# Performance work log

Measured on AMD Instinct MI355X. Metric: run time of the kernel, lower is better.

## Reference

```python
import jax, jax.numpy as jnp
import numpy as np

RADIX = 23                 # hidden_radix fixed-point fractional bits
SCALE = float(1 << RADIX)
F = 10                     # fractional bits used to quantize forget gates
FS = 1 << F
MAX_FORGET = 0.875
H = 512
D = H // 2
SLICE = 100
VOCAB = 32000
T, B = 512, 64
L = 2


def setup_inputs() -> dict:
    key = jax.random.key(0)
    ks = jax.random.split(key, 8)
    s = 0.06  # ~1/sqrt(768) init scale, keeps gates unsaturated
    return {
        "input_seq": jax.random.randint(ks[0], (T, B), 0, VOCAB),
        "lengths": jax.random.randint(ks[1], (B,), 1, T + 1),
        "emb": jax.random.normal(ks[2], (VOCAB, H), jnp.float32) * s,
        "Wz1": jax.random.normal(ks[3], (L, H + D, H), jnp.float32) * s,
        "bz1": jnp.zeros((L, H), jnp.float32),
        "Wg1": jax.random.normal(ks[4], (L, H + D, D), jnp.float32) * s,
        "bg1": jnp.zeros((L, D), jnp.float32),
        "Wz2": jax.random.normal(ks[5], (L, H + D, H), jnp.float32) * s,
        "bz2": jnp.zeros((L, H), jnp.float32),
        "Wg2": jax.random.normal(ks[6], (L, H + D, D), jnp.float32) * s,
        "bg2": jnp.zeros((L, D), jnp.float32),
    }


def _to_float(h_int):
    # ConvertToFloat: dequantize int fixed-point hidden (radix 23)
    return h_int.astype(jnp.float32) / SCALE


def _quant_gate(z):
    # restrict forgetting: z in [1 - max_forget, 1], then quantize to F frac bits
    z = MAX_FORGET * z + (1.0 - MAX_FORGET)
    return jnp.clip(jnp.floor(z * FS), 1, FS).astype(jnp.int32)


def _fixed_mul(h, zq):
    # exact floor(h * zq / 2**F) in int32 (no overflow): split h into hi/lo
    h_hi = h >> F               # arithmetic shift == floor division
    h_lo = h & (FS - 1)
    return h_hi * zq + ((h_lo * zq) >> F)


def _revgru_cell(x, h, Wz1, bz1, Wg1, bg1, Wz2, bz2, Wg2, bg2):
    # h: int32 [B, H] fixed-point hidden, split into reversible halves
    h1, h2 = h[:, :D], h[:, D:]
    h2f = _to_float(h2)
    zr1 = jax.nn.sigmoid(jnp.concatenate([x, h2f], 1) @ Wz1 + bz1)   # [B, H]
    zq1, r1 = _quant_gate(zr1[:, :D]), zr1[:, D:]
    z1f = zq1.astype(jnp.float32) / FS
    g1 = jnp.tanh(jnp.concatenate([x, r1 * h2f], 1) @ Wg1 + bg1)     # [B, D]
    h1 = _fixed_mul(h1, zq1) + jnp.round((1.0 - z1f) * g1 * SCALE).astype(jnp.int32)
    h1f = _to_float(h1)
    zr2 = jax.nn.sigmoid(jnp.concatenate([x, h1f], 1) @ Wz2 + bz2)
    zq2, r2 = _quant_gate(zr2[:, :D]), zr2[:, D:]
    z2f = zq2.astype(jnp.float32) / FS
    g2 = jnp.tanh(jnp.concatenate([x, r2 * h1f], 1) @ Wg2 + bg2)
    h2 = _fixed_mul(h2, zq2) + jnp.round((1.0 - z2f) * g2 * SCALE).astype(jnp.int32)
    return jnp.concatenate([h1, h2], 1)


def reference(input_seq, lengths, emb, Wz1, bz1, Wg1, bg1, Wz2, bz2, Wg2, bg2):
    input_seq = input_seq.astype(jnp.int32)
    xs = emb[input_seq]                                       # [T, B, H] (lockdropi p=0)
    mask = jnp.arange(T)[:, None] < lengths[None, :]          # [T, B]
    h0 = jnp.zeros((B, H), jnp.int32)
    cur = xs
    last_hiddens = []
    all_hs = None
    # stacked RNN: run each layer fully over time (equivalent to the t,l double loop)
    for l in range(L):
        def step(h, inp, l=l):
            x, m = inp
            hn = _revgru_cell(x, h, Wz1[l], bz1[l], Wg1[l], bg1[l],
                              Wz2[l], bz2[l], Wg2[l], bg2[l])
            hn = jnp.where(m[:, None], hn, h)                 # length masking
            return hn, hn
        hT, hs = jax.lax.scan(step, h0, (cur, mask))
        last_hiddens.append(hT)
        if l < L - 1:
            cur = _to_float(hs)                               # output_hidden (lockdroph p=0)
        else:
            all_hs = hs
    # saved_hiddens: top-layer hidden slice before each step plus final -> T+1 entries
    saved = jnp.concatenate([h0[None], all_hs], 0)[:, :, :SLICE]
    return jnp.stack(last_hiddens), saved
```

## Files before the change

### kernel.cpp

```cpp
#include <hip/hip_runtime.h>
#include <stdint.h>


typedef __attribute__((ext_vector_type(8))) short short8;
typedef __attribute__((ext_vector_type(4))) float floatx4;

#define MFMA16(a,b,c) __builtin_amdgcn_mfma_f32_16x16x32_bf16((a),(b),(c),0,0,0)

__device__ __forceinline__ short bf16_rne(float f) {
  uint32_t u = __float_as_uint(f);
  u += 0x7FFFu + ((u >> 16) & 1u);
  return (short)(u >> 16);
}
__device__ __forceinline__ float bf16f(short s) {
  return __uint_as_float(((uint32_t)(uint16_t)s) << 16);
}
__device__ __forceinline__ void st64(unsigned long long* p, unsigned long long v) {
  __hip_atomic_store(p, v, __ATOMIC_RELAXED, __HIP_MEMORY_SCOPE_AGENT);
}
__device__ __forceinline__ unsigned long long ld64(const unsigned long long* p) {
  return __hip_atomic_load(p, __ATOMIC_RELAXED, __HIP_MEMORY_SCOPE_AGENT);
}

#define SCALE_F 8388608.0f
#define INV_S   (1.0f/8388608.0f)

__device__ float g_X[50331648];
__device__ short g_WTh[2][786432];
__device__ short g_WTl[2][786432];
__device__ float g_biasL[2][1536];
__device__ unsigned long long g_ch[2][4][6][4096];
__device__ unsigned long long g_h0s[16777216];
__device__ unsigned long long g_x1r[3145728];
__device__ unsigned long long g_sent[2][4][4][8];
__device__ unsigned g_epoch;

__global__ void bump_epoch() { g_epoch = g_epoch + 1u; }

__global__ void prep_x(const float* __restrict__ Wz1, const float* __restrict__ bz1,
                       const float* __restrict__ Wg1, const float* __restrict__ bg1,
                       const float* __restrict__ Wz2, const float* __restrict__ bz2,
                       const float* __restrict__ Wg2, const float* __restrict__ bg2,
                       int layer, int* __restrict__ d_out, int zero_extra) {
  int idx = blockIdx.x * 256 + threadIdx.x;
  int k = idx / 1536;
  int c = idx - k * 1536;
  const float* W; const float* bb; int cc; int ncols;
  if (c < 512)       { W = Wz1; bb = bz1; cc = c;        ncols = 512; }
  else if (c < 768)  { W = Wg1; bb = bg1; cc = c - 512;  ncols = 256; }
  else if (c < 1280) { W = Wz2; bb = bz2; cc = c - 768;  ncols = 512; }
  else               { W = Wg2; bb = bg2; cc = c - 1280; ncols = 256; }
  float wv = W[(size_t)layer * 768 * ncols + (size_t)k * ncols + cc];
  short hi = bf16_rne(wv);
  short lo = bf16_rne(wv - bf16f(hi));
  g_WTh[layer][(size_t)c * 512 + k] = hi;
  g_WTl[layer][(size_t)c * 512 + k] = lo;
  if (k == 0) g_biasL[layer][c] = bb[layer * ncols + cc];
  if (zero_extra && idx < 6400) d_out[65536 + idx] = 0;
}

__global__ __launch_bounds__(256)
void gemmx_kernel(const int* __restrict__ seq, const float* __restrict__ emb) {
  __shared__ float At[128][36];
  __shared__ short Bhi[128][40];
  __shared__ short Blo[128][40];
  __shared__ int toks[128];
  int tid = threadIdx.x;
  int r0 = blockIdx.x * 128;
  int c0 = blockIdx.y * 128;
  if (tid < 128) toks[tid] = seq[r0 + tid];
  int lane = tid & 63;
  int wid = tid >> 6;
  int wm = wid & 1, wn = wid >> 1;
  int lm = lane & 15, lq = lane >> 4;
  floatx4 zero4 = {0.f, 0.f, 0.f, 0.f};
  floatx4 acc[4][4];
#pragma unroll
  for (int a = 0; a < 4; ++a)
#pragma unroll
    for (int b = 0; b < 4; ++b) acc[a][b] = zero4;
  __syncthreads();
  int am = tid >> 1;
  int ah = (tid & 1) * 16;
  const float* arow = emb + (size_t)toks[am] * 512;
  const short* bh_base = g_WTh[0] + (size_t)(c0 + am) * 512;
  const short* bl_base = g_WTl[0] + (size_t)(c0 + am) * 512;
  for (int kb = 0; kb < 16; ++kb) {
    int k0 = kb * 32 + ah;
    float4 a0 = *(const float4*)(arow + k0);
    float4 a1 = *(const float4*)(arow + k0 + 4);
    float4 a2 = *(const float4*)(arow + k0 + 8);
    float4 a3 = *(const float4*)(arow + k0 + 12);
    short4 b0 = *(const short4*)(bh_base + k0);
    short4 b1 = *(const short4*)(bh_base + k0 + 4);
    short4 b2 = *(const short4*)(bh_base + k0 + 8);
    short4 b3 = *(const short4*)(bh_base + k0 + 12);
    short4 l0 = *(const short4*)(bl_base + k0);
    short4 l1 = *(const short4*)(bl_base + k0 + 4);
    short4 l2 = *(const short4*)(bl_base + k0 + 8);
    short4 l3 = *(const short4*)(bl_base + k0 + 12);
    __syncthreads();
    *(float4*)&At[am][ah]      = a0;
    *(float4*)&At[am][ah + 4]  = a1;
    *(float4*)&At[am][ah + 8]  = a2;
    *(float4*)&At[am][ah + 12] = a3;
    *(short4*)&Bhi[am][ah]      = b0;
    *(short4*)&Bhi[am][ah + 4]  = b1;
    *(short4*)&Bhi[am][ah + 8]  = b2;
    *(short4*)&Bhi[am][ah + 12] = b3;
    *(short4*)&Blo[am][ah]      = l0;
    *(short4*)&Blo[am][ah + 4]  = l1;
    *(short4*)&Blo[am][ah + 8]  = l2;
    *(short4*)&Blo[am][ah + 12] = l3;
    __syncthreads();
    short8 afh[4], afl[4];
#pragma unroll
    for (int mt = 0; mt < 4; ++mt) {
      const float* ap = &At[wm*64 + mt*16 + lm][lq*8];
#pragma unroll
      for (int j = 0; j < 8; ++j) {
        float v = ap[j];
        short hi = bf16_rne(v);
        afh[mt][j] = hi;
        afl[mt][j] = bf16_rne(v - bf16f(hi));
      }
    }
#pragma unroll
    for (int nt = 0; nt < 4; ++nt) {
      short8 bfh = *(short8*)&Bhi[wn*64 + nt*16 + lm][lq*8];
      short8 bfl = *(short8*)&Blo[wn*64 + nt*16 + lm][lq*8];
#pragma unroll
      for (int mt = 0; mt < 4; ++mt) {
        acc[mt][nt] = MFMA16(afh[mt], bfh, acc[mt][nt]);
        acc[mt][nt] = MFMA16(afl[mt], bfh, acc[mt][nt]);
        acc[mt][nt] = MFMA16(afh[mt], bfl, acc[mt][nt]);
      }
    }
  }
#pragma unroll
  for (int nt = 0; nt < 4; ++nt) {
    int gc = c0 + wn*64 + nt*16 + lm;
    float bv = g_biasL[0][gc];
#pragma unroll
    for (int mt = 0; mt < 4; ++mt) {
#pragma unroll
      for (int i = 0; i < 4; ++i) {
        int gr = r0 + wm*64 + mt*16 + lq*4 + i;
        g_X[(size_t)gr * 1536 + gc] = acc[mt][nt][i] + bv;
      }
    }
  }
}

__global__ __launch_bounds__(512, 1)
void fused_kernel(const float* __restrict__ Wz1g, const float* __restrict__ Wg1g,
                  const float* __restrict__ Wz2g, const float* __restrict__ Wg2g,
                  const int* __restrict__ lengths, int* __restrict__ d_out) {
  __shared__ int   h1i[16][260];
  __shared__ int   h2i[16][260];
  __shared__ short phi[16][264];
  __shared__ short pmi[16][264];
  __shared__ short plo[16][264];
  __shared__ float redbuf[2304];
  __shared__ int lens[16];
  __shared__ short ahs[16][520];
  __shared__ short als[16][520];

  int tid = threadIdx.x;
  int bid = blockIdx.x;
  int lane = tid & 63, wv = tid >> 6;
  int lm = lane & 15, lq = lane >> 4;
  unsigned ep = g_epoch;

  if (bid >= 64) {
    int xw = bid - 64;
    int r4 = xw & 3;
    int cs = xw >> 2;
    int colx = cs * 128 + wv * 16 + lm;
    short8 bh[16], bl[16];
#pragma unroll
    for (int kf = 0; kf < 16; ++kf) {
      bh[kf] = *(const short8*)&g_WTh[1][(size_t)colx * 512 + kf * 32 + lq * 8];
      bl[kf] = *(const short8*)&g_WTl[1][(size_t)colx * 512 + kf * 32 + lq * 8];
    }
    float bvx = g_biasL[1][colx];
    int sr2 = tid >> 5;
    int cb  = (tid & 31) * 16;

    for (int t = 0; t < 512; ++t) {
      unsigned tagt = (ep << 10) | (unsigned)(t + 1);
      if (tid < 8) {
        const unsigned long long* sp = &g_sent[0][r4][3][tid];
        while ((int)((unsigned)(ld64(sp) >> 32) - tagt) < 0) __builtin_amdgcn_s_sleep(1);
      }
      __syncthreads();
      {
        const unsigned long long* hp = &g_h0s[((size_t)(t * 64) + r4 * 16 + sr2) * 512 + cb];
        unsigned long long v[16];
        do { v[0] = ld64(hp); } while ((unsigned)(v[0] >> 32) != tagt);
#pragma unroll
        for (int i = 1; i < 16; ++i) v[i] = ld64(hp + i);
        unsigned pend = 0;
#pragma unroll
        for (int i = 1; i < 16; ++i)
          if ((unsigned)(v[i] >> 32) != tagt) pend |= 1u << i;
        while (pend) {
          __builtin_amdgcn_s_sleep(1);
#pragma unroll
          for (int i = 1; i < 16; ++i)
            if (pend & (1u << i)) {
              v[i] = ld64(hp + i);
              if ((unsigned)(v[i] >> 32) == tagt) pend &= ~(1u << i);
            }
        }
#pragma unroll
        for (int i = 0; i < 16; ++i) {
          float f = __uint_as_float((unsigned)v[i]);
          short hi = bf16_rne(f);
          ahs[sr2][cb + i] = hi;
          als[sr2][cb + i] = bf16_rne(f - bf16f(hi));
        }
      }
      __syncthreads();
      floatx4 acc = {0.f, 0.f, 0.f, 0.f};
#pragma unroll
      for (int kf = 0; kf < 16; ++kf) {
        short8 a0 = *(short8*)&ahs[lm][kf * 32 + lq * 8];
        short8 a1 = *(short8*)&als[lm][kf * 32 + lq * 8];
        acc = MFMA16(a0, bh[kf], acc);
        acc = MFMA16(a1, bh[kf], acc);
        acc = MFMA16(a0, bl[kf], acc);
      }
      if (t >= 25) {
        if (tid < 4) {
          unsigned need = (ep << 10) | (unsigned)(t - 24);
          while ((unsigned)(ld64(&g_ch[1][tid][5][0]) >> 32) < need) __builtin_amdgcn_s_sleep(2);
        }
      }
      __syncthreads();
#pragma unroll
      for (int i = 0; i < 4; ++i) {
        int row = r4 * 16 + lq * 4 + i;
        st64(&g_x1r[((size_t)(t & 31) * 64 + row) * 1536 + colx],
             ((unsigned long long)tagt << 32) | __float_as_uint(acc[i] + bvx));
      }
      __syncthreads();
    }
    return;
  }

  int grp = bid & 7;
  int cg  = bid >> 3;
  int L   = grp >> 2;
  int dm  = grp & 3;
  int rb0 = dm * 16;
  unsigned long long (*ch)[4096] = g_ch[L][dm];

  if (tid < 16) lens[tid] = lengths[rb0 + tid];
  for (int i = tid; i < 16 * 260; i += 512) { ((int*)h1i)[i] = 0; ((int*)h2i)[i] = 0; }

  short8 wz1a[4], wz1b[4], wz1c[4], wz2a[4], wz2b[4], wz2c[4];
  short8 wg1a[2], wg1b[2], wg2a[2], wg2b[2];
  {
    int nt = wv & 3, kh = wv >> 2;
    int colz = cg * 64 + nt * 16 + lm;
    const float* W1 = Wz1g + (size_t)L * 768 * 512 + (size_t)512 * 512 + colz;
    const float* W2 = Wz2g + (size_t)L * 768 * 512 + (size_t)512 * 512 + colz;
#pragma unroll
    for (int ks = 0; ks < 4; ++ks) {
      int k0 = kh * 128 + ks * 32 + lq * 8;
      short8 t0, t1, t2, u0, u1, u2;
#pragma unroll
      for (int j = 0; j < 8; ++j) {
        float v = W1[(size_t)(k0 + j) * 512] * INV_S;
        short a0 = bf16_rne(v); float r1 = v - bf16f(a0);
        short a1 = bf16_rne(r1); float r2 = r1 - bf16f(a1);
        t0[j] = a0; t1[j] = a1; t2[j] = bf16_rne(r2);
        float v2 = W2[(size_t)(k0 + j) * 512] * INV_S;
        short d0 = bf16_rne(v2); float s1 = v2 - bf16f(d0);
        short d1 = bf16_rne(s1); float s2 = s1 - bf16f(d1);
        u0[j] = d0; u1[j] = d1; u2[j] = bf16_rne(s2);
      }
      wz1a[ks] = t0; wz1b[ks] = t1; wz1c[ks] = t2;
      wz2a[ks] = u0; wz2b[ks] = u1; wz2c[ks] = u2;
    }
    int ntg = wv & 1, kq = wv >> 1;
    int colg = cg * 32 + ntg * 16 + lm;
    const float* G1 = Wg1g + (size_t)L * 768 * 256 + (size_t)512 * 256 + colg;
    const float* G2 = Wg2g + (size_t)L * 768 * 256 + (size_t)512 * 256 + colg;
#pragma unroll
    for (int ks = 0; ks < 2; ++ks) {
      int k0 = kq * 64 + ks * 32 + lq * 8;
      short8 t0, t1, u0, u1;
#pragma unroll
      for (int j = 0; j < 8; ++j) {
        float v = G1[(size_t)(k0 + j) * 256];
        short a0 = bf16_rne(v);
        t0[j] = a0; t1[j] = bf16_rne(v - bf16f(a0));
        float v2 = G2[(size_t)(k0 + j) * 256];
        short d0 = bf16_rne(v2);
        u0[j] = d0; u1[j] = bf16_rne(v2 - bf16f(d0));
      }
      wg1a[ks] = t0; wg1b[ks] = t1; wg2a[ks] = u0; wg2b[ks] = u1;
    }
  }
  __syncthreads();

  int xr = tid & 15, xc = tid >> 4;
  int sr = tid >> 5, sc0 = (tid & 31) << 3;

  int xo0 = cg * 64 + 2 * xc;
  int xo1 = 512 + cg * 32 + xc;
  int xo2 = 768 + cg * 64 + 2 * xc;
  int xo3 = 1280 + cg * 32 + xc;

  auto ldx = [&](int tt, float& za, float& zb, float& g1x, float& ya, float& yb, float& g2x) {
    const float* base = g_X + (size_t)(tt * 64 + rb0 + xr) * 1536;
    float2 v1 = *(const float2*)(base + cg * 64 + 2 * xc);
    za = v1.x; zb = v1.y;
    g1x = base[512 + cg * 32 + xc];
    float2 v2 = *(const float2*)(base + 768 + cg * 64 + 2 * xc);
    ya = v2.x; yb = v2.y;
    g2x = base[1280 + cg * 32 + xc];
  };
  float cz1a = 0.f, cz1b = 0.f, cg1x = 0.f, cz2a = 0.f, cz2b = 0.f, cg2x = 0.f;
  if (L == 0) ldx(0, cz1a, cz1b, cg1x, cz2a, cz2b, cg2x);

#define GATE(PH, NEED)                                                         \
  {                                                                            \
    if (tid < 8) {                                                             \
      const unsigned long long* sp_ = &g_sent[L][dm][PH][tid];                 \
      while ((int)((unsigned)(ld64(sp_) >> 32) - (NEED)) < 0)                  \
        __builtin_amdgcn_s_sleep(1);                                           \
    }                                                                          \
    __syncthreads();                                                           \
  }

#define STAGE8(CHIDX, EXP, DEPOSIT)                                            \
  {                                                                            \
    const unsigned long long* cp_ = &ch[CHIDX][sr * 256 + sc0];                \
    unsigned long long v_[8];                                                  \
    do { v_[0] = ld64(cp_); } while ((unsigned)(v_[0] >> 32) != (EXP));        \
    _Pragma("unroll")                                                          \
    for (int i_ = 1; i_ < 8; ++i_) v_[i_] = ld64(cp_ + i_);                    \
    unsigned pend_ = 0;                                                        \
    _Pragma("unroll")                                                          \
    for (int i_ = 1; i_ < 8; ++i_)                                             \
      if ((unsigned)(v_[i_] >> 32) != (EXP)) pend_ |= 1u << i_;                \
    while (pend_) {                                                            \
      __builtin_amdgcn_s_sleep(1);                                             \
      _Pragma("unroll")                                                        \
      for (int i_ = 1; i_ < 8; ++i_)                                           \
        if (pend_ & (1u << i_)) {                                              \
          v_[i_] = ld64(cp_ + i_);                                             \
          if ((unsigned)(v_[i_] >> 32) == (EXP)) pend_ &= ~(1u << i_);         \
        }                                                                      \
    }                                                                          \
    _Pragma("unroll")                                                          \
    for (int i_ = 0; i_ < 8; ++i_) { DEPOSIT; }                                \
  }

#define SPLIT3(SRC)                                                            \
  {                                                                            \
    _Pragma("unroll")                                                          \
    for (int i_ = 0; i_ < 8; ++i_) {                                           \
      float v = (float)SRC[sr][sc0 + i_];                                      \
      short a0 = bf16_rne(v); float r1 = v - bf16f(a0);                        \
      short a1 = bf16_rne(r1); float r2 = r1 - bf16f(a1);                      \
      phi[sr][sc0 + i_] = a0; pmi[sr][sc0 + i_] = a1;                          \
      plo[sr][sc0 + i_] = bf16_rne(r2);                                        \
    }                                                                          \
  }

  for (int t = 0; t < 512; ++t) {
    unsigned tagp = (ep << 10) | (unsigned)(t + 1);

    float nz1a, nz1b, ng1x, nz2a, nz2b, ng2x;
    if (L == 0) {
      int tn = (t + 1 < 512) ? t + 1 : t;
      ldx(tn, nz1a, nz1b, ng1x, nz2a, nz2b, ng2x);
    }

    const unsigned long long* xb = nullptr;
    unsigned long long x0v = 0, x1v = 0, x2v = 0, x3v = 0, x4v = 0, x5v = 0;
    if (L == 1) {
      xb = &g_x1r[((size_t)((t & 31) * 64) + rb0 + xr) * 1536];
      x0v = ld64(xb + xo0); x1v = ld64(xb + xo0 + 1);
      x2v = ld64(xb + xo1);
      x3v = ld64(xb + xo2); x4v = ld64(xb + xo2 + 1);
      x5v = ld64(xb + xo3);
    }
    auto vfy = [&](unsigned long long v, const unsigned long long* p) -> float {
      while ((unsigned)(v >> 32) != tagp) { __builtin_amdgcn_s_sleep(1); v = ld64(p); }
      return __uint_as_float((unsigned)v);
    };

    if (t > 0) {
      GATE(3, (ep << 10) | (unsigned)t);
      STAGE8(5, (ep << 10) | (unsigned)t, h2i[sr][sc0 + i_] = (int)(unsigned)v_[i_]);
    }
    SPLIT3(h2i);
    __syncthreads();
    {
      int nt = wv & 3, kh = wv >> 2;
      floatx4 acc = {0.f, 0.f, 0.f, 0.f};
#pragma unroll
      for (int ks = 0; ks < 4; ++ks) {
        int k0 = kh * 128 + ks * 32 + lq * 8;
        short8 a0 = *(short8*)&phi[lm][k0];
        short8 a1 = *(short8*)&pmi[lm][k0];
        short8 a2 = *(short8*)&plo[lm][k0];
        acc = MFMA16(a0, wz1a[ks], acc);
        acc = MFMA16(a0, wz1b[ks], acc);
        acc = MFMA16(a1, wz1a[ks], acc);
        acc = MFMA16(a1, wz1b[ks], acc);
        acc = MFMA16(a0, wz1c[ks], acc);
        acc = MFMA16(a2, wz1a[ks], acc);
      }
#pragma unroll
      for (int i = 0; i < 4; ++i) redbuf[kh * 1088 + (lq * 4 + i) * 68 + nt * 16 + lm] = acc[i];
    }
    __syncthreads();
    {
      if (L == 1) { cz1a = vfy(x0v, xb + xo0); cz1b = vfy(x1v, xb + xo0 + 1); }
#pragma unroll
      for (int u = 0; u < 2; ++u) {
        int cc = 2 * xc + u;
        float pre = redbuf[xr * 68 + cc] + redbuf[1088 + xr * 68 + cc] + (u ? cz1b : cz1a);
        float s = 1.0f / (1.0f + expf(-pre));
        int gcol = cg * 64 + cc;
        if (gcol < 256) {
          float qf = floorf((0.875f * s + 0.125f) * 1024.0f);
          int qi = (int)qf; qi = qi < 1 ? 1 : (qi > 1024 ? 1024 : qi);
          st64(&ch[0][xr * 256 + gcol], ((unsigned long long)tagp << 32) | (unsigned)qi);
        } else {
          int rc = gcol - 256;
          float p = s * ((float)h2i[xr][rc] * INV_S);
          short p0 = bf16_rne(p);
          short p1s = bf16_rne(p - bf16f(p0));
          unsigned pay = ((unsigned)(unsigned short)p0 << 16) | (unsigned)(unsigned short)p1s;
          st64(&ch[1][xr * 256 + rc], ((unsigned long long)tagp << 32) | pay);
        }
      }
    }
    __syncthreads();
    if (tid == 0) st64(&g_sent[L][dm][0][cg], ((unsigned long long)tagp << 32) | 1u);
    GATE(0, tagp);

    int qv;
    STAGE8(1, tagp, { unsigned pl_ = (unsigned)v_[i_];
                      phi[sr][sc0 + i_] = (short)(pl_ >> 16);
                      plo[sr][sc0 + i_] = (short)(pl_ & 0xFFFFu); });
    {
      const unsigned long long* qp = &ch[0][xr * 256 + cg * 32 + xc];
      unsigned long long q64;
      do { q64 = ld64(qp); } while ((unsigned)(q64 >> 32) != tagp);
      qv = (int)(unsigned)q64;
    }
    __syncthreads();
    {
      int ntg = wv & 1, kq = wv >> 1;
      floatx4 acc = {0.f, 0.f, 0.f, 0.f};
#pragma unroll
      for (int ks = 0; ks < 2; ++ks) {
        int k0 = kq * 64 + ks * 32 + lq * 8;
        short8 a0 = *(short8*)&phi[lm][k0];
        short8 a1 = *(short8*)&plo[lm][k0];
        acc = MFMA16(a0, wg1a[ks], acc);
        acc = MFMA16(a1, wg1a[ks], acc);
        acc = MFMA16(a0, wg1b[ks], acc);
      }
#pragma unroll
      for (int i = 0; i < 4; ++i) redbuf[kq * 576 + (lq * 4 + i) * 36 + ntg * 16 + lm] = acc[i];
    }
    __syncthreads();
    {
      if (L == 1) cg1x = vfy(x2v, xb + xo1);
      float pre = redbuf[xr * 36 + xc] + redbuf[576 + xr * 36 + xc]
                + redbuf[1152 + xr * 36 + xc] + redbuf[1728 + xr * 36 + xc] + cg1x;
      float g = tanhf(pre);
      int gc = cg * 32 + xc;
      int q = qv;
      int hold = h1i[xr][gc];
      float zf = (float)q * (1.0f / 1024.0f);
      int ni = (int)rintf((1.0f - zf) * g * SCALE_F);
      int hnew = (hold >> 10) * q + (((hold & 1023) * q) >> 10) + ni;
      if (t >= lens[xr]) hnew = hold;
      st64(&ch[2][xr * 256 + gc], ((unsigned long long)tagp << 32) | (unsigned)hnew);
      if (L == 0)
        st64(&g_h0s[((size_t)(t * 64) + rb0 + xr) * 512 + gc],
             ((unsigned long long)tagp << 32) | __float_as_uint((float)hnew * INV_S));
      else if (gc < 100) d_out[65536 + (t + 1) * 6400 + (rb0 + xr) * 100 + gc] = hnew;
      if (t == 511) d_out[L * 32768 + (rb0 + xr) * 512 + gc] = hnew;
    }
    __syncthreads();
    if (tid == 0) st64(&g_sent[L][dm][1][cg], ((unsigned long long)tagp << 32) | 1u);
    GATE(1, tagp);

    STAGE8(2, tagp, h1i[sr][sc0 + i_] = (int)(unsigned)v_[i_]);
    SPLIT3(h1i);
    __syncthreads();
    {
      int nt = wv & 3, kh = wv >> 2;
      floatx4 acc = {0.f, 0.f, 0.f, 0.f};
#pragma unroll
      for (int ks = 0; ks < 4; ++ks) {
        int k0 = kh * 128 + ks * 32 + lq * 8;
        short8 a0 = *(short8*)&phi[lm][k0];
        short8 a1 = *(short8*)&pmi[lm][k0];
        short8 a2 = *(short8*)&plo[lm][k0];
        acc = MFMA16(a0, wz2a[ks], acc);
        acc = MFMA16(a0, wz2b[ks], acc);
        acc = MFMA16(a1, wz2a[ks], acc);
        acc = MFMA16(a1, wz2b[ks], acc);
        acc = MFMA16(a0, wz2c[ks], acc);
        acc = MFMA16(a2, wz2a[ks], acc);
      }
#pragma unroll
      for (int i = 0; i < 4; ++i) redbuf[kh * 1088 + (lq * 4 + i) * 68 + nt * 16 + lm] = acc[i];
    }
    __syncthreads();
    {
      if (L == 1) { cz2a = vfy(x3v, xb + xo2); cz2b = vfy(x4v, xb + xo2 + 1); }
#pragma unroll
      for (int u = 0; u < 2; ++u) {
        int cc = 2 * xc + u;
        float pre = redbuf[xr * 68 + cc] + redbuf[1088 + xr * 68 + cc] + (u ? cz2b : cz2a);
        float s = 1.0f / (1.0f + expf(-pre));
        int gcol = cg * 64 + cc;
        if (gcol < 256) {
          float qf = floorf((0.875f * s + 0.125f) * 1024.0f);
          int qi = (int)qf; qi = qi < 1 ? 1 : (qi > 1024 ? 1024 : qi);
          st64(&ch[3][xr * 256 + gcol], ((unsigned long long)tagp << 32) | (unsigned)qi);
        } else {
          int rc = gcol - 256;
          float p = s * ((float)h1i[xr][rc] * INV_S);
          short p0 = bf16_rne(p);
          short p1s = bf16_rne(p - bf16f(p0));
          unsigned pay = ((unsigned)(unsigned short)p0 << 16) | (unsigned)(unsigned short)p1s;
          st64(&ch[4][xr * 256 + rc], ((unsigned long long)tagp << 32) | pay);
        }
      }
    }
    __syncthreads();
    if (tid == 0) st64(&g_sent[L][dm][2][cg], ((unsigned long long)tagp << 32) | 1u);
    GATE(2, tagp);

    int qv2;
    STAGE8(4, tagp, { unsigned pl_ = (unsigned)v_[i_];
                      phi[sr][sc0 + i_] = (short)(pl_ >> 16);
                      plo[sr][sc0 + i_] = (short)(pl_ & 0xFFFFu); });
    {
      const unsigned long long* qp = &ch[3][xr * 256 + cg * 32 + xc];
      unsigned long long q64;
      do { q64 = ld64(qp); } while ((unsigned)(q64 >> 32) != tagp);
      qv2 = (int)(unsigned)q64;
    }
    __syncthreads();
    {
      int ntg = wv & 1, kq = wv >> 1;
      floatx4 acc = {0.f, 0.f, 0.f, 0.f};
#pragma unroll
      for (int ks = 0; ks < 2; ++ks) {
        int k0 = kq * 64 + ks * 32 + lq * 8;
        short8 a0 = *(short8*)&phi[lm][k0];
        short8 a1 = *(short8*)&plo[lm][k0];
        acc = MFMA16(a0, wg2a[ks], acc);
        acc = MFMA16(a1, wg2a[ks], acc);
        acc = MFMA16(a0, wg2b[ks], acc);
      }
#pragma unroll
      for (int i = 0; i < 4; ++i) redbuf[kq * 576 + (lq * 4 + i) * 36 + ntg * 16 + lm] = acc[i];
    }
    __syncthreads();
    {
      if (L == 1) cg2x = vfy(x5v, xb + xo3);
      float pre = redbuf[xr * 36 + xc] + redbuf[576 + xr * 36 + xc]
                + redbuf[1152 + xr * 36 + xc] + redbuf[1728 + xr * 36 + xc] + cg2x;
      float g = tanhf(pre);
      int gc = cg * 32 + xc;
      int q = qv2;
      int hold = h2i[xr][gc];
      float zf = (float)q * (1.0f / 1024.0f);
      int ni = (int)rintf((1.0f - zf) * g * SCALE_F);
      int hnew = (hold >> 10) * q + (((hold & 1023) * q) >> 10) + ni;
      if (t >= lens[xr]) hnew = hold;
      st64(&ch[5][xr * 256 + gc], ((unsigned long long)tagp << 32) | (unsigned)hnew);
      if (L == 0)
        st64(&g_h0s[((size_t)(t * 64) + rb0 + xr) * 512 + 256 + gc],
             ((unsigned long long)tagp << 32) | __float_as_uint((float)hnew * INV_S));
      if (t == 511) d_out[L * 32768 + (rb0 + xr) * 512 + 256 + gc] = hnew;
    }
    __syncthreads();
    if (tid == 0) st64(&g_sent[L][dm][3][cg], ((unsigned long long)tagp << 32) | 1u);

    if (L == 0) {
      cz1a = nz1a; cz1b = nz1b; cg1x = ng1x; cz2a = nz2a; cz2b = nz2b; cg2x = ng2x;
    }
  }
#undef GATE
#undef STAGE8
#undef SPLIT3
}

extern "C" void kernel_launch(void* const* d_in, const int* in_sizes, int n_in,
                              void* d_out, int out_size, void* d_ws, size_t ws_size,
                              hipStream_t stream) {
  const int*   seq     = (const int*)d_in[0];
  const int*   lengths = (const int*)d_in[1];
  const float* emb     = (const float*)d_in[2];
  const float* Wz1     = (const float*)d_in[3];
  const float* bz1     = (const float*)d_in[4];
  const float* Wg1     = (const float*)d_in[5];
  const float* bg1     = (const float*)d_in[6];
  const float* Wz2     = (const float*)d_in[7];
  const float* bz2     = (const float*)d_in[8];
  const float* Wg2     = (const float*)d_in[9];
  const float* bg2     = (const float*)d_in[10];
  int* out = (int*)d_out;
  (void)in_sizes; (void)n_in; (void)out_size; (void)d_ws; (void)ws_size;

  bump_epoch<<<1, 1, 0, stream>>>();
  prep_x<<<3072, 256, 0, stream>>>(Wz1, bz1, Wg1, bg1, Wz2, bz2, Wg2, bg2, 0, out, 1);
  prep_x<<<3072, 256, 0, stream>>>(Wz1, bz1, Wg1, bg1, Wz2, bz2, Wg2, bg2, 1, out, 0);
  gemmx_kernel<<<dim3(256, 12), 256, 0, stream>>>(seq, emb);
  fused_kernel<<<112, 512, 0, stream>>>(Wz1, Wg1, Wz2, Wg2, lengths, out);
}
```

Before: 8.532 ms.

## Transpose inter-block exchange buffers to column-major and fuse bf16 split into staging

Changes the layout of the global exchange channels and the h0s buffer from row-major [row][col] to column-major [col][row]. Producer stores from threads with consecutive xr now land on adjacent addresses, and each consumer thread reads one column's 16 rows contiguously. The bf16 three-way split is folded into the staging loop instead of running as a separate pass after it. In exchange the LDS writes become transposed, so shared-memory bank conflicts are possible.

```diff
diff --git a/kernel.cpp b/kernel.cpp
--- a/kernel.cpp
+++ b/kernel.cpp
@@ -184,8 +184,6 @@
       bl[kf] = *(const short8*)&g_WTl[1][(size_t)colx * 512 + kf * 32 + lq * 8];
     }
     float bvx = g_biasL[1][colx];
-    int sr2 = tid >> 5;
-    int cb  = (tid & 31) * 16;
 
     for (int t = 0; t < 512; ++t) {
       unsigned tagt = (ep << 10) | (unsigned)(t + 1);
@@ -195,7 +193,7 @@
       }
       __syncthreads();
       {
-        const unsigned long long* hp = &g_h0s[((size_t)(t * 64) + r4 * 16 + sr2) * 512 + cb];
+        const unsigned long long* hp = &g_h0s[((size_t)t * 512 + tid) * 64 + r4 * 16];
         unsigned long long v[16];
         do { v[0] = ld64(hp); } while ((unsigned)(v[0] >> 32) != tagt);
 #pragma unroll
@@ -217,8 +215,8 @@
         for (int i = 0; i < 16; ++i) {
           float f = __uint_as_float((unsigned)v[i]);
           short hi = bf16_rne(f);
-          ahs[sr2][cb + i] = hi;
-          als[sr2][cb + i] = bf16_rne(f - bf16f(hi));
+          ahs[i][tid] = hi;
+          als[i][tid] = bf16_rne(f - bf16f(hi));
         }
       }
       __syncthreads();
@@ -307,7 +305,7 @@
   __syncthreads();
 
   int xr = tid & 15, xc = tid >> 4;
-  int sr = tid >> 5, sc0 = (tid & 31) << 3;
+  int scc = tid >> 1, sh = (tid & 1) << 3;
 
   int xo0 = cg * 64 + 2 * xc;
   int xo1 = 512 + cg * 32 + xc;
@@ -338,7 +336,7 @@
 
 #define STAGE8(CHIDX, EXP, DEPOSIT)                                            \
   {                                                                            \
-    const unsigned long long* cp_ = &ch[CHIDX][sr * 256 + sc0];                \
+    const unsigned long long* cp_ = &ch[CHIDX][scc * 16 + sh];                 \
     unsigned long long v_[8];                                                  \
     do { v_[0] = ld64(cp_); } while ((unsigned)(v_[0] >> 32) != (EXP));        \
     _Pragma("unroll")                                                          \
@@ -360,15 +358,29 @@
     for (int i_ = 0; i_ < 8; ++i_) { DEPOSIT; }                                \
   }
 
-#define SPLIT3(SRC)                                                            \
+#define DEP_SPLIT(HARR)                                                        \
+  { int hv_ = (int)(unsigned)v_[i_];                                           \
+    HARR[sh + i_][scc] = hv_;                                                  \
+    float fv_ = (float)hv_;                                                    \
+    short a0_ = bf16_rne(fv_); float r1_ = fv_ - bf16f(a0_);                   \
+    short a1_ = bf16_rne(r1_);                                                 \
+    phi[sh + i_][scc] = a0_; pmi[sh + i_][scc] = a1_;                          \
+    plo[sh + i_][scc] = bf16_rne(r1_ - bf16f(a1_)); }
+
+#define DEP_R()                                                                \
+  { unsigned pl_ = (unsigned)v_[i_];                                           \
+    phi[sh + i_][scc] = (short)(pl_ >> 16);                                    \
+    plo[sh + i_][scc] = (short)(pl_ & 0xFFFFu); }
+
+#define SPLIT3Z(SRC)                                                           \
   {                                                                            \
     _Pragma("unroll")                                                          \
     for (int i_ = 0; i_ < 8; ++i_) {                                           \
-      float v = (float)SRC[sr][sc0 + i_];                                      \
+      float v = (float)SRC[sh + i_][scc];                                      \
       short a0 = bf16_rne(v); float r1 = v - bf16f(a0);                        \
-      short a1 = bf16_rne(r1); float r2 = r1 - bf16f(a1);                      \
-      phi[sr][sc0 + i_] = a0; pmi[sr][sc0 + i_] = a1;                          \
-      plo[sr][sc0 + i_] = bf16_rne(r2);                                        \
+      short a1 = bf16_rne(r1);                                                 \
+      phi[sh + i_][scc] = a0; pmi[sh + i_][scc] = a1;                          \
+      plo[sh + i_][scc] = bf16_rne(r1 - bf16f(a1));                            \
     }                                                                          \
   }
 
@@ -397,9 +409,10 @@
 
     if (t > 0) {
       GATE(3, (ep << 10) | (unsigned)t);
-      STAGE8(5, (ep << 10) | (unsigned)t, h2i[sr][sc0 + i_] = (int)(unsigned)v_[i_]);
-    }
-    SPLIT3(h2i);
+      STAGE8(5, (ep << 10) | (unsigned)t, DEP_SPLIT(h2i));
+    } else {
+      SPLIT3Z(h2i);
+    }
     __syncthreads();
     {
       int nt = wv & 3, kh = wv >> 2;
@@ -432,14 +445,14 @@
         if (gcol < 256) {
           float qf = floorf((0.875f * s + 0.125f) * 1024.0f);
           int qi = (int)qf; qi = qi < 1 ? 1 : (qi > 1024 ? 1024 : qi);
-          st64(&ch[0][xr * 256 + gcol], ((unsigned long long)tagp << 32) | (unsigned)qi);
+          st64(&ch[0][gcol * 16 + xr], ((unsigned long long)tagp << 32) | (unsigned)qi);
         } else {
           int rc = gcol - 256;
           float p = s * ((float)h2i[xr][rc] * INV_S);
           short p0 = bf16_rne(p);
           short p1s = bf16_rne(p - bf16f(p0));
           unsigned pay = ((unsigned)(unsigned short)p0 << 16) | (unsigned)(unsigned short)p1s;
-          st64(&ch[1][xr * 256 + rc], ((unsigned long long)tagp << 32) | pay);
+          st64(&ch[1][rc * 16 + xr], ((unsigned long long)tagp << 32) | pay);
         }
       }
     }
@@ -448,11 +461,9 @@
     GATE(0, tagp);
 
     int qv;
-    STAGE8(1, tagp, { unsigned pl_ = (unsigned)v_[i_];
-                      phi[sr][sc0 + i_] = (short)(pl_ >> 16);
-                      plo[sr][sc0 + i_] = (short)(pl_ & 0xFFFFu); });
-    {
-      const unsigned long long* qp = &ch[0][xr * 256 + cg * 32 + xc];
+    STAGE8(1, tagp, DEP_R());
+    {
+      const unsigned long long* qp = &ch[0][(cg * 32 + xc) * 16 + xr];
       unsigned long long q64;
       do { q64 = ld64(qp); } while ((unsigned)(q64 >> 32) != tagp);
       qv = (int)(unsigned)q64;
@@ -486,9 +497,9 @@
       int ni = (int)rintf((1.0f - zf) * g * SCALE_F);
       int hnew = (hold >> 10) * q + (((hold & 1023) * q) >> 10) + ni;
       if (t >= lens[xr]) hnew = hold;
-      st64(&ch[2][xr * 256 + gc], ((unsigned long long)tagp << 32) | (unsigned)hnew);
+      st64(&ch[2][gc * 16 + xr], ((unsigned long long)tagp << 32) | (unsigned)hnew);
       if (L == 0)
-        st64(&g_h0s[((size_t)(t * 64) + rb0 + xr) * 512 + gc],
+        st64(&g_h0s[((size_t)t * 512 + gc) * 64 + rb0 + xr],
              ((unsigned long long)tagp << 32) | __float_as_uint((float)hnew * INV_S));
       else if (gc < 100) d_out[65536 + (t + 1) * 6400 + (rb0 + xr) * 100 + gc] = hnew;
       if (t == 511) d_out[L * 32768 + (rb0 + xr) * 512 + gc] = hnew;
@@ -497,8 +508,7 @@
     if (tid == 0) st64(&g_sent[L][dm][1][cg], ((unsigned long long)tagp << 32) | 1u);
     GATE(1, tagp);
 
-    STAGE8(2, tagp, h1i[sr][sc0 + i_] = (int)(unsigned)v_[i_]);
-    SPLIT3(h1i);
+    STAGE8(2, tagp, DEP_SPLIT(h1i));
     __syncthreads();
     {
       int nt = wv & 3, kh = wv >> 2;
@@ -531,14 +541,14 @@
         if (gcol < 256) {
           float qf = floorf((0.875f * s + 0.125f) * 1024.0f);
           int qi = (int)qf; qi = qi < 1 ? 1 : (qi > 1024 ? 1024 : qi);
-          st64(&ch[3][xr * 256 + gcol], ((unsigned long long)tagp << 32) | (unsigned)qi);
+          st64(&ch[3][gcol * 16 + xr], ((unsigned long long)tagp << 32) | (unsigned)qi);
         } else {
           int rc = gcol - 256;
           float p = s * ((float)h1i[xr][rc] * INV_S);
           short p0 = bf16_rne(p);
           short p1s = bf16_rne(p - bf16f(p0));
           unsigned pay = ((unsigned)(unsigned short)p0 << 16) | (unsigned)(unsigned short)p1s;
-          st64(&ch[4][xr * 256 + rc], ((unsigned long long)tagp << 32) | pay);
+          st64(&ch[4][rc * 16 + xr], ((unsigned long long)tagp << 32) | pay);
         }
       }
     }
@@ -547,11 +557,9 @@
     GATE(2, tagp);
 
     int qv2;
-    STAGE8(4, tagp, { unsigned pl_ = (unsigned)v_[i_];
-                      phi[sr][sc0 + i_] = (short)(pl_ >> 16);
-                      plo[sr][sc0 + i_] = (short)(pl_ & 0xFFFFu); });
-    {
-      const unsigned long long* qp = &ch[3][xr * 256 + cg * 32 + xc];
+    STAGE8(4, tagp, DEP_R());
+    {
+      const unsigned long long* qp = &ch[3][(cg * 32 + xc) * 16 + xr];
       unsigned long long q64;
       do { q64 = ld64(qp); } while ((unsigned)(q64 >> 32) != tagp);
       qv2 = (int)(unsigned)q64;
@@ -585,9 +593,9 @@
       int ni = (int)rintf((1.0f - zf) * g * SCALE_F);
       int hnew = (hold >> 10) * q + (((hold & 1023) * q) >> 10) + ni;
       if (t >= lens[xr]) hnew = hold;
-      st64(&ch[5][xr * 256 + gc], ((unsigned long long)tagp << 32) | (unsigned)hnew);
+      st64(&ch[5][gc * 16 + xr], ((unsigned long long)tagp << 32) | (unsigned)hnew);
       if (L == 0)
-        st64(&g_h0s[((size_t)(t * 64) + rb0 + xr) * 512 + 256 + gc],
+        st64(&g_h0s[((size_t)t * 512 + 256 + gc) * 64 + rb0 + xr],
              ((unsigned long long)tagp << 32) | __float_as_uint((float)hnew * INV_S));
       if (t == 511) d_out[L * 32768 + (rb0 + xr) * 512 + 256 + gc] = hnew;
     }
@@ -600,7 +608,9 @@
   }
 #undef GATE
 #undef STAGE8
-#undef SPLIT3
+#undef DEP_SPLIT
+#undef DEP_R
+#undef SPLIT3Z
 }
 
 extern "C" void kernel_launch(void* const* d_in, const int* in_sizes, int n_in,
```

After: 7.788 ms. 1.1x faster.
